# Kernel tuning notes

Hardware: AMD Instinct MI355X
Metric: run time of the kernel (lower is better)

The kernel has to match this reference:

```python
import jax, jax.numpy as jnp
import numpy as np

N, E, D, H_ATT = 10000, 640000, 128, 64


def setup_inputs() -> dict:
    key = jax.random.key(0)
    ks = jax.random.split(key, 8)
    s = 1.0 / np.sqrt(D)
    return {
        "x": jax.random.normal(ks[0], (N, D), jnp.float32),
        "row": jax.random.randint(ks[1], (E,), 0, N, dtype=jnp.int32),
        "col": jax.random.randint(ks[2], (E,), 0, N, dtype=jnp.int32),
        "W1": jax.random.normal(ks[3], (D, D), jnp.float32) * s,
        "b1": jnp.zeros((D,), jnp.float32),
        "W2": jax.random.normal(ks[4], (D, D), jnp.float32) * s,
        "b2": jnp.zeros((D,), jnp.float32),
        "A1": jax.random.normal(ks[5], (D, H_ATT), jnp.float32) * s,
        "ab1": jnp.zeros((H_ATT,), jnp.float32),
        "A2": jax.random.normal(ks[6], (H_ATT, 1), jnp.float32) * (1.0 / np.sqrt(H_ATT)),
    }


def _cos_sim(a, b):
    # torch.cosine_similarity with eps=1e-8
    num = jnp.sum(a * b, axis=-1)
    den = jnp.maximum(jnp.linalg.norm(a, axis=-1) * jnp.linalg.norm(b, axis=-1), 1e-8)
    return num / den


def _euclid(a, b):
    # nn.PairwiseDistance(p=2)
    return jnp.sqrt(jnp.sum((a - b) ** 2, axis=-1) + 1e-12)


def _gcn(x, ew, row, col, W, b):
    # PyG GCNConv: add self loops (weight 1), symmetric normalization, SpMM.
    n = x.shape[0]
    loop = jnp.arange(n, dtype=row.dtype)
    r = jnp.concatenate([row, loop])  # target
    c = jnp.concatenate([col, loop])  # source
    w = jnp.concatenate([ew, jnp.ones((n,), x.dtype)])
    deg = jax.ops.segment_sum(w, r, num_segments=n)
    dis = jnp.where(deg > 0, jax.lax.rsqrt(jnp.maximum(deg, 1e-12)), 0.0)
    norm = dis[r] * w * dis[c]  # [E+N]
    h = x @ W  # [N, out]
    out = jax.ops.segment_sum(norm[:, None] * h[c], r, num_segments=n)
    return out + b


def reference(x, row, col, W1, b1, W2, b2, A1, ab1, A2):
    # --- cosine branch ---
    w = _cos_sim(x[row], x[col])
    x1 = jax.nn.relu(_gcn(x, w, row, col, W1, b1))
    w = _cos_sim(x1[row], x1[col])
    x1 = _gcn(x1, w, row, col, W2, b2)
    # --- euclidean branch ---
    w = _euclid(x[row], x[col])
    x2 = jax.nn.relu(_gcn(x, w, row, col, W1, b1))
    w = _euclid(x2[row], x2[col])
    x2 = _gcn(x2, w, row, col, W2, b2)
    # --- semantic attention fusion ---
    emb = jnp.stack([x1, x2], axis=1)  # [N, 2, D]
    score = jnp.tanh(emb @ A1 + ab1) @ A2  # [N, 2, 1]
    beta = jax.nn.softmax(score, axis=1)
    return jnp.sum(beta * emb, axis=1)  # [N, D]
```

## Files before the change

### kernel.cpp

```cpp
#include <hip/hip_runtime.h>
#include <cstdint>
#include <cstddef>

#define DF 128
#define HATT 64
#define SL 64
#define RPB 1280

static inline int divup(int a, int b) { return (a + b - 1) / b; }

typedef int vint4 __attribute__((ext_vector_type(4)));

__global__ __launch_bounds__(256) void hist2_kernel(const int* __restrict__ row,
                                                    int* __restrict__ cnt2,
                                                    int E, int n, int ranges, int rpb, int es) {
    int rb = blockIdx.x % ranges;
    int s  = blockIdx.x / ranges;
    int lo = rb * rpb, hi = min(lo + rpb, n);
    int rows = hi - lo;
    __shared__ int lc[RPB];
    for (int j = threadIdx.x; j < rows; j += 256) lc[j] = 0;
    __syncthreads();
    int i0 = s * es, i1 = min(i0 + es, E);
    const vint4* rv = (const vint4*)row;
    for (int j = i0 / 4 + threadIdx.x; j < i1 / 4; j += 256) {
        vint4 r4 = __builtin_nontemporal_load(rv + j);
        if (r4.x >= lo && r4.x < hi) atomicAdd(&lc[r4.x - lo], 1);
        if (r4.y >= lo && r4.y < hi) atomicAdd(&lc[r4.y - lo], 1);
        if (r4.z >= lo && r4.z < hi) atomicAdd(&lc[r4.z - lo], 1);
        if (r4.w >= lo && r4.w < hi) atomicAdd(&lc[r4.w - lo], 1);
    }
    __syncthreads();
    for (int j = threadIdx.x; j < rows; j += 256) cnt2[(size_t)s * n + lo + j] = lc[j];
}

__global__ __launch_bounds__(256) void scanRT_kernel(int* __restrict__ cnt2,
                                                     int* __restrict__ tot, int n) {
    __shared__ int tile[SL][65];
    int r0 = blockIdx.x * 64;
    int w = threadIdx.x >> 6;
    int lane = threadIdx.x & 63;
    int rows = min(64, n - r0);
    for (int s = w; s < SL; s += 4) {
        int v = (lane < rows) ? cnt2[(size_t)s * n + r0 + lane] : 0;
        tile[s][lane] = v;
    }
    __syncthreads();
    int t = threadIdx.x;
    if (t < rows) {
        int run = 0;
#pragma unroll
        for (int s = 0; s < SL; ++s) {
            int v = tile[s][t];
            tile[s][t] = run;
            run += v;
        }
        tot[r0 + t] = run;
    }
    __syncthreads();
    for (int s = w; s < SL; s += 4) {
        if (lane < rows) cnt2[(size_t)s * n + r0 + lane] = tile[s][lane];
    }
}

__global__ __launch_bounds__(1024) void scanT_kernel(const int* __restrict__ tot,
                                                     int* __restrict__ row_ptr, int n) {
    __shared__ int sums[1024];
    int t = threadIdx.x;
    int chunk = (n + 1023) >> 10;
    int start = t * chunk, end = min(start + chunk, n);
    int s = 0;
    for (int r = start; r < end; ++r) s += tot[r];
    sums[t] = s;
    __syncthreads();
    for (int off = 1; off < 1024; off <<= 1) {
        int v = (t >= off) ? sums[t - off] : 0;
        __syncthreads();
        sums[t] += v;
        __syncthreads();
    }
    int run = sums[t] - s;
    for (int r = start; r < end; ++r) {
        row_ptr[r] = run;
        run += tot[r];
    }
    if (t == 1023) row_ptr[n] = sums[1023];
}

__global__ __launch_bounds__(256) void scatter2_kernel(const int* __restrict__ row,
                                                       const int* __restrict__ col,
                                                       const int* __restrict__ cnt2,
                                                       const int* __restrict__ row_ptr,
                                                       unsigned short* __restrict__ col_s,
                                                       int E, int n, int ranges, int rpb, int es) {
    int rb = blockIdx.x % ranges;
    int s  = blockIdx.x / ranges;
    int lo = rb * rpb, hi = min(lo + rpb, n);
    int rows = hi - lo;
    __shared__ int cur[RPB];
    for (int j = threadIdx.x; j < rows; j += 256)
        cur[j] = cnt2[(size_t)s * n + lo + j] + row_ptr[lo + j];
    __syncthreads();
    int i0 = s * es, i1 = min(i0 + es, E);
    const vint4* rv = (const vint4*)row;
    const vint4* cv = (const vint4*)col;
    for (int j = i0 / 4 + threadIdx.x; j < i1 / 4; j += 256) {
        vint4 r4 = __builtin_nontemporal_load(rv + j);
        bool b0 = (r4.x >= lo && r4.x < hi);
        bool b1 = (r4.y >= lo && r4.y < hi);
        bool b2 = (r4.z >= lo && r4.z < hi);
        bool b3 = (r4.w >= lo && r4.w < hi);
        if (b0 | b1 | b2 | b3) {
            vint4 c4 = __builtin_nontemporal_load(cv + j);
            if (b0) { int p = atomicAdd(&cur[r4.x - lo], 1); col_s[p] = (unsigned short)c4.x; }
            if (b1) { int p = atomicAdd(&cur[r4.y - lo], 1); col_s[p] = (unsigned short)c4.y; }
            if (b2) { int p = atomicAdd(&cur[r4.z - lo], 1); col_s[p] = (unsigned short)c4.z; }
            if (b3) { int p = atomicAdd(&cur[r4.w - lo], 1); col_s[p] = (unsigned short)c4.w; }
        }
    }
}

__global__ __launch_bounds__(256) void split_x_kernel(const float* __restrict__ x,
                                                      float* __restrict__ xA,
                                                      float* __restrict__ xB,
                                                      float* __restrict__ sqn, int n) {
    int wid = (blockIdx.x * blockDim.x + threadIdx.x) >> 6;
    int lane = threadIdx.x & 63;
    if (wid >= n) return;
    float v0 = x[(size_t)wid * DF + lane];
    float v1 = x[(size_t)wid * DF + 64 + lane];
    xA[(size_t)wid * 64 + lane] = v0;
    xB[(size_t)wid * 64 + lane] = v1;
    float s = v0 * v0 + v1 * v1;
    for (int off = 32; off; off >>= 1) s += __shfl_xor(s, off);
    if (lane == 0) sqn[wid] = s;
}


__global__ __launch_bounds__(256) void edgewA_kernel(const float* __restrict__ tA,
                                                     const unsigned short* __restrict__ col_s,
                                                     const int* __restrict__ row_ptr,
                                                     float* __restrict__ dpart, int n) {
    int wid = (blockIdx.x * blockDim.x + threadIdx.x) >> 6;
    int lane = threadIdx.x & 63;
    if (wid >= n) return;
    int sub = lane & 15, g = lane >> 4;
    int s = row_ptr[wid], e = row_ptr[wid + 1];
    float4 a = ((const float4*)(tA + (size_t)wid * 64))[sub];
    for (int base = s; base < e; base += 64) {
        int m = e - base; if (m > 64) m = 64;
        int cc = 0;
        if (lane < m) cc = (int)col_s[base + lane];
        float dkeep = 0.f;
#define EWA_BODY(CHK)                                                        \
        _Pragma("unroll")                                                    \
        for (int it = 0; it < 16; ++it) {                                    \
            int idx = g * 16 + it;                                           \
            int c = __shfl(cc, idx);                                         \
            if (CHK) {                                                       \
                float4 b = ((const float4*)(tA + (size_t)c * 64))[sub];      \
                float d = a.x * b.x + a.y * b.y + a.z * b.z + a.w * b.w;     \
                d += __shfl_xor(d, 8); d += __shfl_xor(d, 4);                \
                d += __shfl_xor(d, 2); d += __shfl_xor(d, 1);                \
                dkeep = (sub == it) ? d : dkeep;                             \
            }                                                                \
        }
        if (m == 64) { EWA_BODY(true) } else { EWA_BODY(idx < m) }
#undef EWA_BODY
        if (lane < m) dpart[base + lane] = dkeep;
    }
}

__global__ __launch_bounds__(256) void edgewB1_kernel(const float* __restrict__ tB,
                                                      const float* __restrict__ sqn,
                                                      const unsigned short* __restrict__ col_s,
                                                      const int* __restrict__ row_ptr,
                                                      const float* __restrict__ dpart,
                                                      float* __restrict__ wA,
                                                      float* __restrict__ wB,
                                                      float* __restrict__ disA,
                                                      float* __restrict__ disB, int n) {
    int wid = (blockIdx.x * blockDim.x + threadIdx.x) >> 6;
    int lane = threadIdx.x & 63;
    if (wid >= n) return;
    int sub = lane & 15, g = lane >> 4;
    int s = row_ptr[wid], e = row_ptr[wid + 1];
    float4 a = ((const float4*)(tB + (size_t)wid * 64))[sub];
    float na = sqn[wid];
    float accA = 0.f, accB = 0.f;
    for (int base = s; base < e; base += 64) {
        int m = e - base; if (m > 64) m = 64;
        int cc = 0; float dp = 0.f;
        if (lane < m) {
            cc = (int)col_s[base + lane];
            dp = dpart[base + lane];
        }
        float dkeep = 0.f;
#define EWB1_BODY(CHK)                                                       \
        _Pragma("unroll")                                                    \
        for (int it = 0; it < 16; ++it) {                                    \
            int idx = g * 16 + it;                                           \
            int c = __shfl(cc, idx);                                         \
            if (CHK) {                                                       \
                float4 b = ((const float4*)(tB + (size_t)c * 64))[sub];      \
                float d = a.x * b.x + a.y * b.y + a.z * b.z + a.w * b.w;     \
                d += __shfl_xor(d, 8); d += __shfl_xor(d, 4);                \
                d += __shfl_xor(d, 2); d += __shfl_xor(d, 1);                \
                dkeep = (sub == it) ? d : dkeep;                             \
            }                                                                \
        }
        if (m == 64) { EWB1_BODY(true) } else { EWB1_BODY(idx < m) }
#undef EWB1_BODY
        if (lane < m) {
            float d = dkeep + dp;
            float nb = sqn[cc];
            float cw = d / fmaxf(sqrtf(na * nb), 1e-8f);
            float ew = sqrtf(fmaxf(na + nb - 2.f * d, 0.f) + 1e-12f);
            wA[base + lane] = cw;
            wB[base + lane] = ew;
            accA += cw;
            accB += ew;
        }
    }
#pragma unroll
    for (int off = 32; off; off >>= 1) {
        accA += __shfl_xor(accA, off);
        accB += __shfl_xor(accB, off);
    }
    if (lane == 0) {
        float dA = 1.f + accA;
        disA[wid] = (dA > 0.f) ? rsqrtf(fmaxf(dA, 1e-12f)) : 0.f;
        float dB = 1.f + accB;
        disB[wid] = (dB > 0.f) ? rsqrtf(fmaxf(dB, 1e-12f)) : 0.f;
    }
}

__global__ __launch_bounds__(256) void edgewA2_kernel(const float* __restrict__ t0,
                                                      const float* __restrict__ t1,
                                                      const unsigned short* __restrict__ col_s,
                                                      const int* __restrict__ row_ptr,
                                                      float* __restrict__ dp0,
                                                      float* __restrict__ dp1, int n) {
    int br = blockIdx.x & 1;
    int wid = (blockIdx.x >> 1) * 4 + (threadIdx.x >> 6);
    int lane = threadIdx.x & 63;
    if (wid >= n) return;
    const float* tA = br ? t1 : t0;
    float* dpart = br ? dp1 : dp0;
    int sub = lane & 15, g = lane >> 4;
    int s = row_ptr[wid], e = row_ptr[wid + 1];
    float4 a = ((const float4*)(tA + (size_t)wid * 64))[sub];
    for (int base = s; base < e; base += 64) {
        int m = e - base; if (m > 64) m = 64;
        int cc = 0;
        if (lane < m) cc = (int)col_s[base + lane];
        float dkeep = 0.f;
#define EWA2_BODY(CHK)                                                       \
        _Pragma("unroll")                                                    \
        for (int it = 0; it < 16; ++it) {                                    \
            int idx = g * 16 + it;                                           \
            int c = __shfl(cc, idx);                                         \
            if (CHK) {                                                       \
                float4 b = ((const float4*)(tA + (size_t)c * 64))[sub];      \
                float d = a.x * b.x + a.y * b.y + a.z * b.z + a.w * b.w;     \
                d += __shfl_xor(d, 8); d += __shfl_xor(d, 4);                \
                d += __shfl_xor(d, 2); d += __shfl_xor(d, 1);                \
                dkeep = (sub == it) ? d : dkeep;                             \
            }                                                                \
        }
        if (m == 64) { EWA2_BODY(true) } else { EWA2_BODY(idx < m) }
#undef EWA2_BODY
        if (lane < m) dpart[base + lane] = dkeep;
    }
}

__global__ __launch_bounds__(256) void edgewB2_kernel(const float* __restrict__ t0B,
                                                      const float* __restrict__ t1B,
                                                      const float* __restrict__ sq1pA,
                                                      const float* __restrict__ sq1pB,
                                                      const float* __restrict__ sq2pA,
                                                      const float* __restrict__ sq2pB,
                                                      const unsigned short* __restrict__ col_s,
                                                      const int* __restrict__ row_ptr,
                                                      const float* __restrict__ dp0,
                                                      const float* __restrict__ dp1,
                                                      float* __restrict__ wsA,
                                                      float* __restrict__ wsB,
                                                      float* __restrict__ disA,
                                                      float* __restrict__ disB, int n) {
    int br = blockIdx.x & 1;
    int wid = (blockIdx.x >> 1) * 4 + (threadIdx.x >> 6);
    int lane = threadIdx.x & 63;
    if (wid >= n) return;
    const float* tB = br ? t1B : t0B;
    const float* sqA = br ? sq2pA : sq1pA;
    const float* sqB = br ? sq2pB : sq1pB;
    const float* dpart = br ? dp1 : dp0;
    float* wOut = br ? wsB : wsA;
    float* disOut = br ? disB : disA;
    int sub = lane & 15, g = lane >> 4;
    int s = row_ptr[wid], e = row_ptr[wid + 1];
    float4 a = ((const float4*)(tB + (size_t)wid * 64))[sub];
    float na = sqA[wid] + sqB[wid];
    float acc = 0.f;
    for (int base = s; base < e; base += 64) {
        int m = e - base; if (m > 64) m = 64;
        int cc = 0; float dp = 0.f;
        if (lane < m) {
            cc = (int)col_s[base + lane];
            dp = dpart[base + lane];
        }
        float dkeep = 0.f;
#define EWB2_BODY(CHK)                                                       \
        _Pragma("unroll")                                                    \
        for (int it = 0; it < 16; ++it) {                                    \
            int idx = g * 16 + it;                                           \
            int c = __shfl(cc, idx);                                         \
            if (CHK) {                                                       \
                float4 b = ((const float4*)(tB + (size_t)c * 64))[sub];      \
                float d = a.x * b.x + a.y * b.y + a.z * b.z + a.w * b.w;     \
                d += __shfl_xor(d, 8); d += __shfl_xor(d, 4);                \
                d += __shfl_xor(d, 2); d += __shfl_xor(d, 1);                \
                dkeep = (sub == it) ? d : dkeep;                             \
            }                                                                \
        }
        if (m == 64) { EWB2_BODY(true) } else { EWB2_BODY(idx < m) }
#undef EWB2_BODY
        if (lane < m) {
            float d = dkeep + dp;
            float nb = sqA[cc] + sqB[cc];
            float w;
            if (br == 0) w = d / fmaxf(sqrtf(na * nb), 1e-8f);
            else w = sqrtf(fmaxf(na + nb - 2.f * d, 0.f) + 1e-12f);
            wOut[base + lane] = w;
            acc += w;
        }
    }
#pragma unroll
    for (int off = 32; off; off >>= 1) acc += __shfl_xor(acc, off);
    if (lane == 0) {
        float dg = 1.f + acc;
        disOut[wid] = (dg > 0.f) ? rsqrtf(fmaxf(dg, 1e-12f)) : 0.f;
    }
}

__global__ __launch_bounds__(256) void mm_kernel(const float* __restrict__ inA,
                                                 const float* __restrict__ inB,
                                                 int strideIn,
                                                 const float* __restrict__ W,
                                                 float* __restrict__ hA,
                                                 float* __restrict__ hB, int n) {
    int wid = (blockIdx.x * blockDim.x + threadIdx.x) >> 6;
    int lane = threadIdx.x & 63;
    int i0 = wid * 4;
    if (i0 >= n) return;
    float v0[4], v1[4];
#pragma unroll
    for (int r = 0; r < 4; ++r) {
        int i = i0 + r;
        if (i < n) { v0[r] = inA[(size_t)i * strideIn + lane]; v1[r] = inB[(size_t)i * strideIn + lane]; }
        else { v0[r] = 0.f; v1[r] = 0.f; }
    }
    float acc0[4] = {0.f, 0.f, 0.f, 0.f};
    float acc1[4] = {0.f, 0.f, 0.f, 0.f};
#pragma unroll 4
    for (int k = 0; k < 64; ++k) {
        float w0 = W[k * DF + lane];
        float w1 = W[k * DF + 64 + lane];
#pragma unroll
        for (int r = 0; r < 4; ++r) {
            float a = __shfl(v0[r], k);
            acc0[r] = fmaf(a, w0, acc0[r]);
            acc1[r] = fmaf(a, w1, acc1[r]);
        }
    }
#pragma unroll 4
    for (int k = 0; k < 64; ++k) {
        float w0 = W[(k + 64) * DF + lane];
        float w1 = W[(k + 64) * DF + 64 + lane];
#pragma unroll
        for (int r = 0; r < 4; ++r) {
            float a = __shfl(v1[r], k);
            acc0[r] = fmaf(a, w0, acc0[r]);
            acc1[r] = fmaf(a, w1, acc1[r]);
        }
    }
#pragma unroll
    for (int r = 0; r < 4; ++r) {
        int i = i0 + r;
        if (i < n) { hA[(size_t)i * 64 + lane] = acc0[r]; hB[(size_t)i * 64 + lane] = acc1[r]; }
    }
}

__global__ __launch_bounds__(256) void mm2_kernel(const float* __restrict__ x1A_,
                                                  const float* __restrict__ x1B_,
                                                  const float* __restrict__ x2A_,
                                                  const float* __restrict__ x2B_,
                                                  const float* __restrict__ W,
                                                  float* __restrict__ h1A, float* __restrict__ h1B,
                                                  float* __restrict__ h2A, float* __restrict__ h2B,
                                                  int n) {
    int br = blockIdx.x & 1;
    const float* inA = br ? x2A_ : x1A_;
    const float* inB = br ? x2B_ : x1B_;
    float* hA = br ? h2A : h1A;
    float* hB = br ? h2B : h1B;
    int wid = (blockIdx.x >> 1) * 4 + (threadIdx.x >> 6);
    int lane = threadIdx.x & 63;
    int i0 = wid * 4;
    if (i0 >= n) return;
    float v0[4], v1[4];
#pragma unroll
    for (int r = 0; r < 4; ++r) {
        int i = i0 + r;
        if (i < n) { v0[r] = inA[(size_t)i * 64 + lane]; v1[r] = inB[(size_t)i * 64 + lane]; }
        else { v0[r] = 0.f; v1[r] = 0.f; }
    }
    float acc0[4] = {0.f, 0.f, 0.f, 0.f};
    float acc1[4] = {0.f, 0.f, 0.f, 0.f};
#pragma unroll 4
    for (int k = 0; k < 64; ++k) {
        float w0 = W[k * DF + lane];
        float w1 = W[k * DF + 64 + lane];
#pragma unroll
        for (int r = 0; r < 4; ++r) {
            float a = __shfl(v0[r], k);
            acc0[r] = fmaf(a, w0, acc0[r]);
            acc1[r] = fmaf(a, w1, acc1[r]);
        }
    }
#pragma unroll 4
    for (int k = 0; k < 64; ++k) {
        float w0 = W[(k + 64) * DF + lane];
        float w1 = W[(k + 64) * DF + 64 + lane];
#pragma unroll
        for (int r = 0; r < 4; ++r) {
            float a = __shfl(v1[r], k);
            acc0[r] = fmaf(a, w0, acc0[r]);
            acc1[r] = fmaf(a, w1, acc1[r]);
        }
    }
#pragma unroll
    for (int r = 0; r < 4; ++r) {
        int i = i0 + r;
        if (i < n) { hA[(size_t)i * 64 + lane] = acc0[r]; hB[(size_t)i * 64 + lane] = acc1[r]; }
    }
}

__global__ __launch_bounds__(256) void spmm_l1_kernel(const float* __restrict__ hA,
                                                      const float* __restrict__ hB,
                                                      const float* __restrict__ wsA,
                                                      const float* __restrict__ wsB,
                                                      const unsigned short* __restrict__ col_s,
                                                      const float* __restrict__ disA,
                                                      const float* __restrict__ disB,
                                                      const int* __restrict__ row_ptr,
                                                      const float* __restrict__ bias,
                                                      float* __restrict__ x1A, float* __restrict__ x1B,
                                                      float* __restrict__ x2A, float* __restrict__ x2B,
                                                      float* __restrict__ sq1pA, float* __restrict__ sq1pB,
                                                      float* __restrict__ sq2pA, float* __restrict__ sq2pB,
                                                      int n) {
    int half = blockIdx.x & 1;
    int wid = (blockIdx.x >> 1) * 4 + (threadIdx.x >> 6);
    int lane = threadIdx.x & 63;
    if (wid >= n) return;
    const float* hH = half ? hB : hA;
    float* x1H = half ? x1B : x1A;
    float* x2H = half ? x2B : x2A;
    float* sq1 = half ? sq1pB : sq1pA;
    float* sq2 = half ? sq2pB : sq2pA;
    const float* biasH = bias + half * 64;
    int sub = lane & 15, g = lane >> 4;
    int s = row_ptr[wid], e = row_ptr[wid + 1];
    float diA = disA[wid], diB = disB[wid];
    float4 aA = make_float4(0.f, 0.f, 0.f, 0.f);
    float4 aB = make_float4(0.f, 0.f, 0.f, 0.f);
    for (int base = s; base < e; base += 64) {
        int m = e - base; if (m > 64) m = 64;
        int cc = 0; float wa = 0.f, wb = 0.f;
        if (lane < m) {
            cc = (int)col_s[base + lane];
            wa = wsA[base + lane] * disA[cc];
            wb = wsB[base + lane] * disB[cc];
        }
#define SPL1_BODY(CHK)                                                       \
        _Pragma("unroll")                                                    \
        for (int it = 0; it < 16; ++it) {                                    \
            int idx = it * 4 + g;                                            \
            int c = __shfl(cc, idx);                                         \
            float ceA = __shfl(wa, idx);                                     \
            float ceB = __shfl(wb, idx);                                     \
            if (CHK) {                                                       \
                float4 gv = ((const float4*)(hH + (size_t)c * 64))[sub];     \
                aA.x = fmaf(ceA, gv.x, aA.x); aA.y = fmaf(ceA, gv.y, aA.y);  \
                aA.z = fmaf(ceA, gv.z, aA.z); aA.w = fmaf(ceA, gv.w, aA.w);  \
                aB.x = fmaf(ceB, gv.x, aB.x); aB.y = fmaf(ceB, gv.y, aB.y);  \
                aB.z = fmaf(ceB, gv.z, aB.z); aB.w = fmaf(ceB, gv.w, aB.w);  \
            }                                                                \
        }
        if (m == 64) { SPL1_BODY(true) } else { SPL1_BODY(idx < m) }
#undef SPL1_BODY
    }
#pragma unroll
    for (int off = 16; off <= 32; off <<= 1) {
        aA.x += __shfl_xor(aA.x, off); aA.y += __shfl_xor(aA.y, off);
        aA.z += __shfl_xor(aA.z, off); aA.w += __shfl_xor(aA.w, off);
        aB.x += __shfl_xor(aB.x, off); aB.y += __shfl_xor(aB.y, off);
        aB.z += __shfl_xor(aB.z, off); aB.w += __shfl_xor(aB.w, off);
    }
    float4 hv = ((const float4*)(hH + (size_t)wid * 64))[sub];
    float4 bb = ((const float4*)biasH)[sub];
    float4 oA, oB;
    oA.x = fmaxf(diA * (aA.x + diA * hv.x) + bb.x, 0.f);
    oA.y = fmaxf(diA * (aA.y + diA * hv.y) + bb.y, 0.f);
    oA.z = fmaxf(diA * (aA.z + diA * hv.z) + bb.z, 0.f);
    oA.w = fmaxf(diA * (aA.w + diA * hv.w) + bb.w, 0.f);
    oB.x = fmaxf(diB * (aB.x + diB * hv.x) + bb.x, 0.f);
    oB.y = fmaxf(diB * (aB.y + diB * hv.y) + bb.y, 0.f);
    oB.z = fmaxf(diB * (aB.z + diB * hv.z) + bb.z, 0.f);
    oB.w = fmaxf(diB * (aB.w + diB * hv.w) + bb.w, 0.f);
    if (g == 0) {
        ((float4*)(x1H + (size_t)wid * 64))[sub] = oA;
        ((float4*)(x2H + (size_t)wid * 64))[sub] = oB;
    }
    float sA = oA.x * oA.x + oA.y * oA.y + oA.z * oA.z + oA.w * oA.w;
    float sB = oB.x * oB.x + oB.y * oB.y + oB.z * oB.z + oB.w * oB.w;
#pragma unroll
    for (int off = 8; off; off >>= 1) {
        sA += __shfl_xor(sA, off);
        sB += __shfl_xor(sB, off);
    }
    if (lane == 0) { sq1[wid] = sA; sq2[wid] = sB; }
}

__global__ __launch_bounds__(256) void spmm2q_kernel(const float* __restrict__ h1A,
                                                     const float* __restrict__ h1B,
                                                     const float* __restrict__ h2A,
                                                     const float* __restrict__ h2B,
                                                     const float* __restrict__ wsA,
                                                     const float* __restrict__ wsB,
                                                     const unsigned short* __restrict__ col_s,
                                                     const float* __restrict__ disA,
                                                     const float* __restrict__ disB,
                                                     const int* __restrict__ row_ptr,
                                                     const float* __restrict__ bias,
                                                     float* __restrict__ x1A, float* __restrict__ x1B,
                                                     float* __restrict__ x2A, float* __restrict__ x2B,
                                                     int n) {
    int sel = blockIdx.x & 3;
    int br = sel & 1;
    int half = sel >> 1;
    const float* hH = br ? (half ? h2B : h2A) : (half ? h1B : h1A);
    const float* ws = br ? wsB : wsA;
    const float* dis = br ? disB : disA;
    float* outH = br ? (half ? x2B : x2A) : (half ? x1B : x1A);
    const float* biasH = bias + half * 64;
    int wid = (blockIdx.x >> 2) * 4 + (threadIdx.x >> 6);
    int lane = threadIdx.x & 63;
    if (wid >= n) return;
    int sub = lane & 15, g = lane >> 4;
    int s = row_ptr[wid], e = row_ptr[wid + 1];
    float di = dis[wid];
    float4 a = make_float4(0.f, 0.f, 0.f, 0.f);
    for (int base = s; base < e; base += 64) {
        int m = e - base; if (m > 64) m = 64;
        int cc = 0; float wv = 0.f;
        if (lane < m) {
            cc = (int)col_s[base + lane];
            wv = ws[base + lane] * dis[cc];
        }
#define SP2_BODY(CHK)                                                        \
        _Pragma("unroll")                                                    \
        for (int it = 0; it < 16; ++it) {                                    \
            int idx = it * 4 + g;                                            \
            int c = __shfl(cc, idx);                                         \
            float ce = __shfl(wv, idx);                                      \
            if (CHK) {                                                       \
                float4 gv = ((const float4*)(hH + (size_t)c * 64))[sub];     \
                a.x = fmaf(ce, gv.x, a.x); a.y = fmaf(ce, gv.y, a.y);        \
                a.z = fmaf(ce, gv.z, a.z); a.w = fmaf(ce, gv.w, a.w);        \
            }                                                                \
        }
        if (m == 64) { SP2_BODY(true) } else { SP2_BODY(idx < m) }
#undef SP2_BODY
    }
#pragma unroll
    for (int off = 16; off <= 32; off <<= 1) {
        a.x += __shfl_xor(a.x, off); a.y += __shfl_xor(a.y, off);
        a.z += __shfl_xor(a.z, off); a.w += __shfl_xor(a.w, off);
    }
    if (g == 0) {
        float4 hv = ((const float4*)(hH + (size_t)wid * 64))[sub];
        float4 bb = ((const float4*)biasH)[sub];
        float4 o;
        o.x = di * (a.x + di * hv.x) + bb.x;
        o.y = di * (a.y + di * hv.y) + bb.y;
        o.z = di * (a.z + di * hv.z) + bb.z;
        o.w = di * (a.w + di * hv.w) + bb.w;
        ((float4*)(outH + (size_t)wid * 64))[sub] = o;
    }
}

__global__ __launch_bounds__(256) void attn_kernel(const float* __restrict__ x1A,
                                                   const float* __restrict__ x1B,
                                                   const float* __restrict__ x2A,
                                                   const float* __restrict__ x2B,
                                                   const float* __restrict__ A1,
                                                   const float* __restrict__ ab1,
                                                   const float* __restrict__ A2,
                                                   float* __restrict__ out, int n) {
    __shared__ float sA1[DF * HATT];
    __shared__ float sA2[HATT];
    __shared__ float sab[HATT];
    int tid = threadIdx.x;
    for (int i = tid; i < DF * HATT; i += 256) sA1[i] = A1[i];
    if (tid < HATT) { sA2[tid] = A2[tid]; sab[tid] = ab1[tid]; }
    __syncthreads();
    int lane = tid & 63;
    int wib = tid >> 6;
    int wid = blockIdx.x * 4 + wib;
    int nw = gridDim.x * 4;
    for (int i = wid; i < n; i += nw) {
        float u0 = x1A[(size_t)i * 64 + lane], u1 = x1B[(size_t)i * 64 + lane];
        float v0 = x2A[(size_t)i * 64 + lane], v1 = x2B[(size_t)i * 64 + lane];
        float acc1 = 0.f, acc2 = 0.f;
#pragma unroll 4
        for (int d = 0; d < 64; ++d) {
            float w = sA1[d * HATT + lane];
            acc1 = fmaf(__shfl(u0, d), w, acc1);
            acc2 = fmaf(__shfl(v0, d), w, acc2);
        }
#pragma unroll 4
        for (int d = 0; d < 64; ++d) {
            float w = sA1[(d + 64) * HATT + lane];
            acc1 = fmaf(__shfl(u1, d), w, acc1);
            acc2 = fmaf(__shfl(v1, d), w, acc2);
        }
        float t1 = tanhf(acc1 + sab[lane]) * sA2[lane];
        float t2 = tanhf(acc2 + sab[lane]) * sA2[lane];
        for (int off = 32; off; off >>= 1) {
            t1 += __shfl_xor(t1, off);
            t2 += __shfl_xor(t2, off);
        }
        float mx = fmaxf(t1, t2);
        float e1 = expf(t1 - mx), e2 = expf(t2 - mx);
        float inv = 1.f / (e1 + e2);
        float be1 = e1 * inv, be2 = e2 * inv;
        out[(size_t)i * DF + lane] = be1 * u0 + be2 * v0;
        out[(size_t)i * DF + 64 + lane] = be1 * u1 + be2 * v1;
    }
}


extern "C" void kernel_launch(void* const* d_in, const int* in_sizes, int n_in,
                              void* d_out, int out_size, void* d_ws, size_t ws_size,
                              hipStream_t stream) {
    const float* x  = (const float*)d_in[0];
    const int* row  = (const int*)d_in[1];
    const int* col  = (const int*)d_in[2];
    const float* W1 = (const float*)d_in[3];
    const float* b1 = (const float*)d_in[4];
    const float* W2 = (const float*)d_in[5];
    const float* b2 = (const float*)d_in[6];
    const float* A1 = (const float*)d_in[7];
    const float* ab1= (const float*)d_in[8];
    const float* A2 = (const float*)d_in[9];
    const int N = in_sizes[0] / DF;
    const int E = in_sizes[1];
    float* out = (float*)d_out;

    char* p = (char*)d_ws;
    auto alloc_b = [&](size_t bytes) -> char* {
        char* r = p;
        p += (bytes + 255) & ~(size_t)255;
        return r;
    };
    float* xA    = (float*)alloc_b((size_t)N * 64 * 4);
    float* xB    = (float*)alloc_b((size_t)N * 64 * 4);
    float* hA    = (float*)alloc_b((size_t)N * 64 * 4);
    float* hB    = (float*)alloc_b((size_t)N * 64 * 4);
    float* h2A   = (float*)alloc_b((size_t)N * 64 * 4);
    float* h2B   = (float*)alloc_b((size_t)N * 64 * 4);
    float* x1A   = (float*)alloc_b((size_t)N * 64 * 4);
    float* x1B   = (float*)alloc_b((size_t)N * 64 * 4);
    float* x2A   = (float*)alloc_b((size_t)N * 64 * 4);
    float* x2B   = (float*)alloc_b((size_t)N * 64 * 4);
    float* wsA   = (float*)alloc_b((size_t)E * 4);
    float* wsB   = (float*)alloc_b((size_t)E * 4);
    float* dp0   = (float*)alloc_b((size_t)E * 4);
    float* dp1   = (float*)alloc_b((size_t)E * 4);
    float* disA  = (float*)alloc_b((size_t)N * 4);
    float* disB  = (float*)alloc_b((size_t)N * 4);
    float* sqnx  = (float*)alloc_b((size_t)N * 4);
    float* sq1pA = (float*)alloc_b((size_t)N * 4);
    float* sq1pB = (float*)alloc_b((size_t)N * 4);
    float* sq2pA = (float*)alloc_b((size_t)N * 4);
    float* sq2pB = (float*)alloc_b((size_t)N * 4);
    int* cnt2    = (int*)alloc_b((size_t)SL * N * 4);
    int* tot     = (int*)alloc_b((size_t)N * 4);
    int* rowptr  = (int*)alloc_b((size_t)(N + 1) * 4);
    unsigned short* col_s = (unsigned short*)alloc_b((size_t)E * 2);
    (void)ws_size; (void)n_in; (void)out_size;

    const int nodeBlocks  = divup(N * 64, 256);
    const int pairBlocks  = 2 * nodeBlocks;
    const int quadBlocks  = 4 * nodeBlocks;
    const int mmBlocks    = divup(divup(N, 4), 4);
    const int mm2Blocks   = 2 * mmBlocks;
    const int ranges = divup(N, RPB);
    const int rpb    = divup(N, ranges);
    int es = divup(E, SL); es = (es + 3) & ~3;
    const int prepBlocks = ranges * SL;

    hist2_kernel<<<prepBlocks, 256, 0, stream>>>(row, cnt2, E, N, ranges, rpb, es);
    split_x_kernel<<<nodeBlocks, 256, 0, stream>>>(x, xA, xB, sqnx, N);
    scanRT_kernel<<<divup(N, 64), 256, 0, stream>>>(cnt2, tot, N);
    scanT_kernel<<<1, 1024, 0, stream>>>(tot, rowptr, N);
    scatter2_kernel<<<prepBlocks, 256, 0, stream>>>(row, col, cnt2, rowptr, col_s, E, N, ranges, rpb, es);

    mm_kernel<<<mmBlocks, 256, 0, stream>>>(x, x + 64, DF, W1, hA, hB, N);

    edgewA_kernel<<<nodeBlocks, 256, 0, stream>>>(xA, col_s, rowptr, dp0, N);
    edgewB1_kernel<<<nodeBlocks, 256, 0, stream>>>(xB, sqnx, col_s, rowptr, dp0,
                                                   wsA, wsB, disA, disB, N);

    spmm_l1_kernel<<<pairBlocks, 256, 0, stream>>>(hA, hB, wsA, wsB, col_s, disA, disB,
                                                   rowptr, b1, x1A, x1B, x2A, x2B,
                                                   sq1pA, sq1pB, sq2pA, sq2pB, N);

    edgewA2_kernel<<<pairBlocks, 256, 0, stream>>>(x1A, x2A, col_s, rowptr, dp0, dp1, N);
    edgewB2_kernel<<<pairBlocks, 256, 0, stream>>>(x1B, x2B, sq1pA, sq1pB, sq2pA, sq2pB,
                                                   col_s, rowptr, dp0, dp1,
                                                   wsA, wsB, disA, disB, N);

    mm2_kernel<<<mm2Blocks, 256, 0, stream>>>(x1A, x1B, x2A, x2B, W2, hA, hB, h2A, h2B, N);

    spmm2q_kernel<<<quadBlocks, 256, 0, stream>>>(hA, hB, h2A, h2B, wsA, wsB, col_s,
                                                  disA, disB, rowptr, b2,
                                                  x1A, x1B, x2A, x2B, N);

    attn_kernel<<<divup(N, 4), 256, 0, stream>>>(x1A, x1B, x2A, x2B, A1, ab1, A2, out, N);
}
```

Baseline: 358.1 us.

## Store GCN hidden features in bf16 and unify SpMM kernels over full rows

The matmul outputs h (x@W1, x1/x2@W2) are now written as interleaved bf16 rows of 128 features instead of two fp32 half-buffers. A single templated SpMM kernel gathers full 256-byte bf16 rows per neighbour and handles both feature halves per wave. This halves gather traffic and removes the quad-launch split. A new scale_wd pass pre-multiplies edge weights by dis[col], so the SpMM no longer does that lookup per edge. Squared norms are now produced as one value per node. The cost is bf16 rounding of the hidden features, which lowers accuracy, plus two extra lightweight elementwise launches.

```diff
diff --git a/kernel.cpp b/kernel.cpp
--- a/kernel.cpp
+++ b/kernel.cpp
@@ -10,6 +10,18 @@
 static inline int divup(int a, int b) { return (a + b - 1) / b; }
 
 typedef int vint4 __attribute__((ext_vector_type(4)));
+typedef unsigned short vus8 __attribute__((ext_vector_type(8)));
+
+struct U16x4 { unsigned short x, y, z, w; };
+
+static __device__ __forceinline__ unsigned short f2bf(float f) {
+    unsigned int u = __float_as_uint(f);
+    u = (u + 0x7FFFu + ((u >> 16) & 1u)) >> 16;
+    return (unsigned short)u;
+}
+static __device__ __forceinline__ float bf2f(unsigned short b) {
+    return __uint_as_float(((unsigned int)b) << 16);
+}
 
 __global__ __launch_bounds__(256) void hist2_kernel(const int* __restrict__ row,
                                                     int* __restrict__ cnt2,
@@ -136,7 +148,6 @@
     if (lane == 0) sqn[wid] = s;
 }
 
-
 __global__ __launch_bounds__(256) void edgewA_kernel(const float* __restrict__ tA,
                                                      const unsigned short* __restrict__ col_s,
                                                      const int* __restrict__ row_ptr,
@@ -276,10 +287,8 @@
 
 __global__ __launch_bounds__(256) void edgewB2_kernel(const float* __restrict__ t0B,
                                                       const float* __restrict__ t1B,
-                                                      const float* __restrict__ sq1pA,
-                                                      const float* __restrict__ sq1pB,
-                                                      const float* __restrict__ sq2pA,
-                                                      const float* __restrict__ sq2pB,
+                                                      const float* __restrict__ sqn1,
+                                                      const float* __restrict__ sqn2,
                                                       const unsigned short* __restrict__ col_s,
                                                       const int* __restrict__ row_ptr,
                                                       const float* __restrict__ dp0,
@@ -293,15 +302,14 @@
     int lane = threadIdx.x & 63;
     if (wid >= n) return;
     const float* tB = br ? t1B : t0B;
-    const float* sqA = br ? sq2pA : sq1pA;
-    const float* sqB = br ? sq2pB : sq1pB;
+    const float* sq = br ? sqn2 : sqn1;
     const float* dpart = br ? dp1 : dp0;
     float* wOut = br ? wsB : wsA;
     float* disOut = br ? disB : disA;
     int sub = lane & 15, g = lane >> 4;
     int s = row_ptr[wid], e = row_ptr[wid + 1];
     float4 a = ((const float4*)(tB + (size_t)wid * 64))[sub];
-    float na = sqA[wid] + sqB[wid];
+    float na = sq[wid];
     float acc = 0.f;
     for (int base = s; base < e; base += 64) {
         int m = e - base; if (m > 64) m = 64;
@@ -328,7 +336,7 @@
 #undef EWB2_BODY
         if (lane < m) {
             float d = dkeep + dp;
-            float nb = sqA[cc] + sqB[cc];
+            float nb = sq[cc];
             float w;
             if (br == 0) w = d / fmaxf(sqrtf(na * nb), 1e-8f);
             else w = sqrtf(fmaxf(na + nb - 2.f * d, 0.f) + 1e-12f);
@@ -344,12 +352,27 @@
     }
 }
 
+__global__ __launch_bounds__(256) void scale_wd_kernel(float* __restrict__ wsA,
+                                                       float* __restrict__ wsB,
+                                                       const unsigned short* __restrict__ col_s,
+                                                       const float* __restrict__ disA,
+                                                       const float* __restrict__ disB, int E4) {
+    int j = blockIdx.x * 256 + threadIdx.x;
+    if (j >= E4) return;
+    U16x4 c4 = ((const U16x4*)col_s)[j];
+    float4 wa = ((const float4*)wsA)[j];
+    float4 wb = ((const float4*)wsB)[j];
+    wa.x *= disA[c4.x]; wa.y *= disA[c4.y]; wa.z *= disA[c4.z]; wa.w *= disA[c4.w];
+    wb.x *= disB[c4.x]; wb.y *= disB[c4.y]; wb.z *= disB[c4.z]; wb.w *= disB[c4.w];
+    ((float4*)wsA)[j] = wa;
+    ((float4*)wsB)[j] = wb;
+}
+
 __global__ __launch_bounds__(256) void mm_kernel(const float* __restrict__ inA,
                                                  const float* __restrict__ inB,
                                                  int strideIn,
                                                  const float* __restrict__ W,
-                                                 float* __restrict__ hA,
-                                                 float* __restrict__ hB, int n) {
+                                                 unsigned short* __restrict__ hab, int n) {
     int wid = (blockIdx.x * blockDim.x + threadIdx.x) >> 6;
     int lane = threadIdx.x & 63;
     int i0 = wid * 4;
@@ -388,7 +411,10 @@
 #pragma unroll
     for (int r = 0; r < 4; ++r) {
         int i = i0 + r;
-        if (i < n) { hA[(size_t)i * 64 + lane] = acc0[r]; hB[(size_t)i * 64 + lane] = acc1[r]; }
+        if (i < n) {
+            hab[(size_t)i * DF + lane] = f2bf(acc0[r]);
+            hab[(size_t)i * DF + 64 + lane] = f2bf(acc1[r]);
+        }
     }
 }
 
@@ -397,14 +423,12 @@
                                                   const float* __restrict__ x2A_,
                                                   const float* __restrict__ x2B_,
                                                   const float* __restrict__ W,
-                                                  float* __restrict__ h1A, float* __restrict__ h1B,
-                                                  float* __restrict__ h2A, float* __restrict__ h2B,
-                                                  int n) {
+                                                  unsigned short* __restrict__ h1ab,
+                                                  unsigned short* __restrict__ h2ab, int n) {
     int br = blockIdx.x & 1;
     const float* inA = br ? x2A_ : x1A_;
     const float* inB = br ? x2B_ : x1B_;
-    float* hA = br ? h2A : h1A;
-    float* hB = br ? h2B : h1B;
+    unsigned short* hab = br ? h2ab : h1ab;
     int wid = (blockIdx.x >> 1) * 4 + (threadIdx.x >> 6);
     int lane = threadIdx.x & 63;
     int i0 = wid * 4;
@@ -443,162 +467,108 @@
 #pragma unroll
     for (int r = 0; r < 4; ++r) {
         int i = i0 + r;
-        if (i < n) { hA[(size_t)i * 64 + lane] = acc0[r]; hB[(size_t)i * 64 + lane] = acc1[r]; }
-    }
-}
-
-__global__ __launch_bounds__(256) void spmm_l1_kernel(const float* __restrict__ hA,
-                                                      const float* __restrict__ hB,
-                                                      const float* __restrict__ wsA,
-                                                      const float* __restrict__ wsB,
-                                                      const unsigned short* __restrict__ col_s,
-                                                      const float* __restrict__ disA,
-                                                      const float* __restrict__ disB,
-                                                      const int* __restrict__ row_ptr,
-                                                      const float* __restrict__ bias,
-                                                      float* __restrict__ x1A, float* __restrict__ x1B,
-                                                      float* __restrict__ x2A, float* __restrict__ x2B,
-                                                      float* __restrict__ sq1pA, float* __restrict__ sq1pB,
-                                                      float* __restrict__ sq2pA, float* __restrict__ sq2pB,
-                                                      int n) {
-    int half = blockIdx.x & 1;
+        if (i < n) {
+            hab[(size_t)i * DF + lane] = f2bf(acc0[r]);
+            hab[(size_t)i * DF + 64 + lane] = f2bf(acc1[r]);
+        }
+    }
+}
+
+template <int RELU>
+__global__ __launch_bounds__(256) void spmm_kernel(const unsigned short* __restrict__ hab0,
+                                                   const unsigned short* __restrict__ hab1,
+                                                   const float* __restrict__ wd0,
+                                                   const float* __restrict__ wd1,
+                                                   const unsigned short* __restrict__ col_s,
+                                                   const float* __restrict__ dis0,
+                                                   const float* __restrict__ dis1,
+                                                   const int* __restrict__ row_ptr,
+                                                   const float* __restrict__ bias,
+                                                   float* __restrict__ o0A, float* __restrict__ o0B,
+                                                   float* __restrict__ o1A, float* __restrict__ o1B,
+                                                   float* __restrict__ sq0, float* __restrict__ sq1,
+                                                   int n) {
+    int br = blockIdx.x & 1;
+    const unsigned short* hab = br ? hab1 : hab0;
+    const float* wd = br ? wd1 : wd0;
+    const float* disp = br ? dis1 : dis0;
+    float* outA = br ? o1A : o0A;
+    float* outB = br ? o1B : o0B;
     int wid = (blockIdx.x >> 1) * 4 + (threadIdx.x >> 6);
-    int lane = threadIdx.x & 63;
-    if (wid >= n) return;
-    const float* hH = half ? hB : hA;
-    float* x1H = half ? x1B : x1A;
-    float* x2H = half ? x2B : x2A;
-    float* sq1 = half ? sq1pB : sq1pA;
-    float* sq2 = half ? sq2pB : sq2pA;
-    const float* biasH = bias + half * 64;
-    int sub = lane & 15, g = lane >> 4;
-    int s = row_ptr[wid], e = row_ptr[wid + 1];
-    float diA = disA[wid], diB = disB[wid];
-    float4 aA = make_float4(0.f, 0.f, 0.f, 0.f);
-    float4 aB = make_float4(0.f, 0.f, 0.f, 0.f);
-    for (int base = s; base < e; base += 64) {
-        int m = e - base; if (m > 64) m = 64;
-        int cc = 0; float wa = 0.f, wb = 0.f;
-        if (lane < m) {
-            cc = (int)col_s[base + lane];
-            wa = wsA[base + lane] * disA[cc];
-            wb = wsB[base + lane] * disB[cc];
-        }
-#define SPL1_BODY(CHK)                                                       \
-        _Pragma("unroll")                                                    \
-        for (int it = 0; it < 16; ++it) {                                    \
-            int idx = it * 4 + g;                                            \
-            int c = __shfl(cc, idx);                                         \
-            float ceA = __shfl(wa, idx);                                     \
-            float ceB = __shfl(wb, idx);                                     \
-            if (CHK) {                                                       \
-                float4 gv = ((const float4*)(hH + (size_t)c * 64))[sub];     \
-                aA.x = fmaf(ceA, gv.x, aA.x); aA.y = fmaf(ceA, gv.y, aA.y);  \
-                aA.z = fmaf(ceA, gv.z, aA.z); aA.w = fmaf(ceA, gv.w, aA.w);  \
-                aB.x = fmaf(ceB, gv.x, aB.x); aB.y = fmaf(ceB, gv.y, aB.y);  \
-                aB.z = fmaf(ceB, gv.z, aB.z); aB.w = fmaf(ceB, gv.w, aB.w);  \
-            }                                                                \
-        }
-        if (m == 64) { SPL1_BODY(true) } else { SPL1_BODY(idx < m) }
-#undef SPL1_BODY
-    }
-#pragma unroll
-    for (int off = 16; off <= 32; off <<= 1) {
-        aA.x += __shfl_xor(aA.x, off); aA.y += __shfl_xor(aA.y, off);
-        aA.z += __shfl_xor(aA.z, off); aA.w += __shfl_xor(aA.w, off);
-        aB.x += __shfl_xor(aB.x, off); aB.y += __shfl_xor(aB.y, off);
-        aB.z += __shfl_xor(aB.z, off); aB.w += __shfl_xor(aB.w, off);
-    }
-    float4 hv = ((const float4*)(hH + (size_t)wid * 64))[sub];
-    float4 bb = ((const float4*)biasH)[sub];
-    float4 oA, oB;
-    oA.x = fmaxf(diA * (aA.x + diA * hv.x) + bb.x, 0.f);
-    oA.y = fmaxf(diA * (aA.y + diA * hv.y) + bb.y, 0.f);
-    oA.z = fmaxf(diA * (aA.z + diA * hv.z) + bb.z, 0.f);
-    oA.w = fmaxf(diA * (aA.w + diA * hv.w) + bb.w, 0.f);
-    oB.x = fmaxf(diB * (aB.x + diB * hv.x) + bb.x, 0.f);
-    oB.y = fmaxf(diB * (aB.y + diB * hv.y) + bb.y, 0.f);
-    oB.z = fmaxf(diB * (aB.z + diB * hv.z) + bb.z, 0.f);
-    oB.w = fmaxf(diB * (aB.w + diB * hv.w) + bb.w, 0.f);
-    if (g == 0) {
-        ((float4*)(x1H + (size_t)wid * 64))[sub] = oA;
-        ((float4*)(x2H + (size_t)wid * 64))[sub] = oB;
-    }
-    float sA = oA.x * oA.x + oA.y * oA.y + oA.z * oA.z + oA.w * oA.w;
-    float sB = oB.x * oB.x + oB.y * oB.y + oB.z * oB.z + oB.w * oB.w;
-#pragma unroll
-    for (int off = 8; off; off >>= 1) {
-        sA += __shfl_xor(sA, off);
-        sB += __shfl_xor(sB, off);
-    }
-    if (lane == 0) { sq1[wid] = sA; sq2[wid] = sB; }
-}
-
-__global__ __launch_bounds__(256) void spmm2q_kernel(const float* __restrict__ h1A,
-                                                     const float* __restrict__ h1B,
-                                                     const float* __restrict__ h2A,
-                                                     const float* __restrict__ h2B,
-                                                     const float* __restrict__ wsA,
-                                                     const float* __restrict__ wsB,
-                                                     const unsigned short* __restrict__ col_s,
-                                                     const float* __restrict__ disA,
-                                                     const float* __restrict__ disB,
-                                                     const int* __restrict__ row_ptr,
-                                                     const float* __restrict__ bias,
-                                                     float* __restrict__ x1A, float* __restrict__ x1B,
-                                                     float* __restrict__ x2A, float* __restrict__ x2B,
-                                                     int n) {
-    int sel = blockIdx.x & 3;
-    int br = sel & 1;
-    int half = sel >> 1;
-    const float* hH = br ? (half ? h2B : h2A) : (half ? h1B : h1A);
-    const float* ws = br ? wsB : wsA;
-    const float* dis = br ? disB : disA;
-    float* outH = br ? (half ? x2B : x2A) : (half ? x1B : x1A);
-    const float* biasH = bias + half * 64;
-    int wid = (blockIdx.x >> 2) * 4 + (threadIdx.x >> 6);
     int lane = threadIdx.x & 63;
     if (wid >= n) return;
     int sub = lane & 15, g = lane >> 4;
     int s = row_ptr[wid], e = row_ptr[wid + 1];
-    float di = dis[wid];
-    float4 a = make_float4(0.f, 0.f, 0.f, 0.f);
+    float di = disp[wid];
+    float acc[8];
+#pragma unroll
+    for (int j = 0; j < 8; ++j) acc[j] = 0.f;
     for (int base = s; base < e; base += 64) {
         int m = e - base; if (m > 64) m = 64;
         int cc = 0; float wv = 0.f;
         if (lane < m) {
             cc = (int)col_s[base + lane];
-            wv = ws[base + lane] * dis[cc];
-        }
-#define SP2_BODY(CHK)                                                        \
+            wv = wd[base + lane];
+        }
+#define SPM_BODY(CHK)                                                        \
         _Pragma("unroll")                                                    \
         for (int it = 0; it < 16; ++it) {                                    \
             int idx = it * 4 + g;                                            \
             int c = __shfl(cc, idx);                                         \
             float ce = __shfl(wv, idx);                                      \
             if (CHK) {                                                       \
-                float4 gv = ((const float4*)(hH + (size_t)c * 64))[sub];     \
-                a.x = fmaf(ce, gv.x, a.x); a.y = fmaf(ce, gv.y, a.y);        \
-                a.z = fmaf(ce, gv.z, a.z); a.w = fmaf(ce, gv.w, a.w);        \
+                vus8 gv = ((const vus8*)(hab + (size_t)c * DF))[sub];        \
+                _Pragma("unroll")                                            \
+                for (int j = 0; j < 8; ++j)                                  \
+                    acc[j] = fmaf(ce, bf2f(gv[j]), acc[j]);                  \
             }                                                                \
         }
-        if (m == 64) { SP2_BODY(true) } else { SP2_BODY(idx < m) }
-#undef SP2_BODY
+        if (m == 64) { SPM_BODY(true) } else { SPM_BODY(idx < m) }
+#undef SPM_BODY
     }
 #pragma unroll
     for (int off = 16; off <= 32; off <<= 1) {
-        a.x += __shfl_xor(a.x, off); a.y += __shfl_xor(a.y, off);
-        a.z += __shfl_xor(a.z, off); a.w += __shfl_xor(a.w, off);
+#pragma unroll
+        for (int j = 0; j < 8; ++j) acc[j] += __shfl_xor(acc[j], off);
+    }
+    vus8 hv = ((const vus8*)(hab + (size_t)wid * DF))[sub];
+    float4 bbl = ((const float4*)bias)[sub * 2];
+    float4 bbh = ((const float4*)bias)[sub * 2 + 1];
+    float o[8];
+    o[0] = di * (acc[0] + di * bf2f(hv[0])) + bbl.x;
+    o[1] = di * (acc[1] + di * bf2f(hv[1])) + bbl.y;
+    o[2] = di * (acc[2] + di * bf2f(hv[2])) + bbl.z;
+    o[3] = di * (acc[3] + di * bf2f(hv[3])) + bbl.w;
+    o[4] = di * (acc[4] + di * bf2f(hv[4])) + bbh.x;
+    o[5] = di * (acc[5] + di * bf2f(hv[5])) + bbh.y;
+    o[6] = di * (acc[6] + di * bf2f(hv[6])) + bbh.z;
+    o[7] = di * (acc[7] + di * bf2f(hv[7])) + bbh.w;
+    if (RELU) {
+#pragma unroll
+        for (int j = 0; j < 8; ++j) o[j] = fmaxf(o[j], 0.f);
     }
     if (g == 0) {
-        float4 hv = ((const float4*)(hH + (size_t)wid * 64))[sub];
-        float4 bb = ((const float4*)biasH)[sub];
-        float4 o;
-        o.x = di * (a.x + di * hv.x) + bb.x;
-        o.y = di * (a.y + di * hv.y) + bb.y;
-        o.z = di * (a.z + di * hv.z) + bb.z;
-        o.w = di * (a.w + di * hv.w) + bb.w;
-        ((float4*)(outH + (size_t)wid * 64))[sub] = o;
+        float4 lo = make_float4(o[0], o[1], o[2], o[3]);
+        float4 hi = make_float4(o[4], o[5], o[6], o[7]);
+        if (sub < 8) {
+            ((float4*)(outA + (size_t)wid * 64))[sub * 2] = lo;
+            ((float4*)(outA + (size_t)wid * 64))[sub * 2 + 1] = hi;
+        } else {
+            int sb = sub - 8;
+            ((float4*)(outB + (size_t)wid * 64))[sb * 2] = lo;
+            ((float4*)(outB + (size_t)wid * 64))[sb * 2 + 1] = hi;
+        }
+    }
+    if (RELU) {
+        float* sq = br ? sq1 : sq0;
+        float ss = 0.f;
+#pragma unroll
+        for (int j = 0; j < 8; ++j) ss = fmaf(o[j], o[j], ss);
+        ss += __shfl_xor(ss, 8);
+        ss += __shfl_xor(ss, 4);
+        ss += __shfl_xor(ss, 2);
+        ss += __shfl_xor(ss, 1);
+        if (lane == 0) sq[wid] = ss;
     }
 }
 
@@ -678,10 +648,8 @@
     };
     float* xA    = (float*)alloc_b((size_t)N * 64 * 4);
     float* xB    = (float*)alloc_b((size_t)N * 64 * 4);
-    float* hA    = (float*)alloc_b((size_t)N * 64 * 4);
-    float* hB    = (float*)alloc_b((size_t)N * 64 * 4);
-    float* h2A   = (float*)alloc_b((size_t)N * 64 * 4);
-    float* h2B   = (float*)alloc_b((size_t)N * 64 * 4);
+    unsigned short* hab  = (unsigned short*)alloc_b((size_t)N * DF * 2);
+    unsigned short* h2ab = (unsigned short*)alloc_b((size_t)N * DF * 2);
     float* x1A   = (float*)alloc_b((size_t)N * 64 * 4);
     float* x1B   = (float*)alloc_b((size_t)N * 64 * 4);
     float* x2A   = (float*)alloc_b((size_t)N * 64 * 4);
@@ -693,10 +661,8 @@
     float* disA  = (float*)alloc_b((size_t)N * 4);
     float* disB  = (float*)alloc_b((size_t)N * 4);
     float* sqnx  = (float*)alloc_b((size_t)N * 4);
-    float* sq1pA = (float*)alloc_b((size_t)N * 4);
-    float* sq1pB = (float*)alloc_b((size_t)N * 4);
-    float* sq2pA = (float*)alloc_b((size_t)N * 4);
-    float* sq2pB = (float*)alloc_b((size_t)N * 4);
+    float* sqn1  = (float*)alloc_b((size_t)N * 4);
+    float* sqn2  = (float*)alloc_b((size_t)N * 4);
     int* cnt2    = (int*)alloc_b((size_t)SL * N * 4);
     int* tot     = (int*)alloc_b((size_t)N * 4);
     int* rowptr  = (int*)alloc_b((size_t)(N + 1) * 4);
@@ -705,9 +671,9 @@
 
     const int nodeBlocks  = divup(N * 64, 256);
     const int pairBlocks  = 2 * nodeBlocks;
-    const int quadBlocks  = 4 * nodeBlocks;
     const int mmBlocks    = divup(divup(N, 4), 4);
     const int mm2Blocks   = 2 * mmBlocks;
+    const int vecBlocks   = divup(E / 4, 256);
     const int ranges = divup(N, RPB);
     const int rpb    = divup(N, ranges);
     int es = divup(E, SL); es = (es + 3) & ~3;
@@ -719,26 +685,28 @@
     scanT_kernel<<<1, 1024, 0, stream>>>(tot, rowptr, N);
     scatter2_kernel<<<prepBlocks, 256, 0, stream>>>(row, col, cnt2, rowptr, col_s, E, N, ranges, rpb, es);
 
-    mm_kernel<<<mmBlocks, 256, 0, stream>>>(x, x + 64, DF, W1, hA, hB, N);
+    mm_kernel<<<mmBlocks, 256, 0, stream>>>(x, x + 64, DF, W1, hab, N);
 
     edgewA_kernel<<<nodeBlocks, 256, 0, stream>>>(xA, col_s, rowptr, dp0, N);
     edgewB1_kernel<<<nodeBlocks, 256, 0, stream>>>(xB, sqnx, col_s, rowptr, dp0,
                                                    wsA, wsB, disA, disB, N);
-
-    spmm_l1_kernel<<<pairBlocks, 256, 0, stream>>>(hA, hB, wsA, wsB, col_s, disA, disB,
+    scale_wd_kernel<<<vecBlocks, 256, 0, stream>>>(wsA, wsB, col_s, disA, disB, E / 4);
+
+    spmm_kernel<1><<<pairBlocks, 256, 0, stream>>>(hab, hab, wsA, wsB, col_s, disA, disB,
                                                    rowptr, b1, x1A, x1B, x2A, x2B,
-                                                   sq1pA, sq1pB, sq2pA, sq2pB, N);
+                                                   sqn1, sqn2, N);
 
     edgewA2_kernel<<<pairBlocks, 256, 0, stream>>>(x1A, x2A, col_s, rowptr, dp0, dp1, N);
-    edgewB2_kernel<<<pairBlocks, 256, 0, stream>>>(x1B, x2B, sq1pA, sq1pB, sq2pA, sq2pB,
+    edgewB2_kernel<<<pairBlocks, 256, 0, stream>>>(x1B, x2B, sqn1, sqn2,
                                                    col_s, rowptr, dp0, dp1,
                                                    wsA, wsB, disA, disB, N);
-
-    mm2_kernel<<<mm2Blocks, 256, 0, stream>>>(x1A, x1B, x2A, x2B, W2, hA, hB, h2A, h2B, N);
-
-    spmm2q_kernel<<<quadBlocks, 256, 0, stream>>>(hA, hB, h2A, h2B, wsA, wsB, col_s,
-                                                  disA, disB, rowptr, b2,
-                                                  x1A, x1B, x2A, x2B, N);
+    scale_wd_kernel<<<vecBlocks, 256, 0, stream>>>(wsA, wsB, col_s, disA, disB, E / 4);
+
+    mm2_kernel<<<mm2Blocks, 256, 0, stream>>>(x1A, x1B, x2A, x2B, W2, hab, h2ab, N);
+
+    spmm_kernel<0><<<pairBlocks, 256, 0, stream>>>(hab, h2ab, wsA, wsB, col_s, disA, disB,
+                                                   rowptr, b2, x1A, x1B, x2A, x2B,
+                                                   sqn1, sqn2, N);
 
     attn_kernel<<<divup(N, 4), 256, 0, stream>>>(x1A, x1B, x2A, x2B, A1, ab1, A2, out, N);
 }
```

New measurement: 351.1 us. About the same (-1.9%).
